# Optimization experiments

Hardware: AMD Instinct MI355X
Metric: run time of the kernel (lower is better)

Reference implementation:

```python
import jax, jax.numpy as jnp
import numpy as np

V, D, N, T, U, E = 200000, 128, 50000, 20, 128, 128

def setup_inputs() -> dict:
    key = jax.random.key(0)
    ks = jax.random.split(key, 12)
    s = 0.02
    return {
        "node_ids": jax.random.randint(ks[0], (N,), 0, V, dtype=jnp.int32),
        "neigh_ids": jax.random.randint(ks[1], (N, T), 0, V, dtype=jnp.int32),
        "alpha": jax.random.uniform(ks[2], (N, T), dtype=jnp.float32),
        "table": jax.random.normal(ks[3], (V, D), dtype=jnp.float32),
        "Wq": jax.random.normal(ks[4], (D, U), dtype=jnp.float32) * s,
        "bq": jnp.zeros((U,), dtype=jnp.float32),
        "Wn": jax.random.normal(ks[5], (D, U), dtype=jnp.float32) * s,
        "bn": jnp.zeros((U,), dtype=jnp.float32),
        "Ww": jax.random.normal(ks[6], (2 * U, U), dtype=jnp.float32) * s,
        "bw": jnp.zeros((U,), dtype=jnp.float32),
        "Wg": jax.random.normal(ks[7], (U, E), dtype=jnp.float32) * s,
        "bg": jnp.zeros((E,), dtype=jnp.float32),
    }

def reference(node_ids, neigh_ids, alpha, table, Wq, bq, Wn, bn, Ww, bw, Wg, bg):
    # gather initial embeddings (irregular indexing)
    node_x = table[node_ids]            # [N, D]
    neigh_x = table[neigh_ids]          # [N, T, D]
    # Convolve: node branch Dense+ReLU
    node_h = jax.nn.relu(node_x @ Wq + bq)                       # [N, U]
    # Aggregator: neighbor Dense+ReLU then alpha-weighted matmul
    neigh_h = jax.nn.relu(jnp.einsum('ntd,du->ntu', neigh_x, Wn) + bn)  # [N, T, U]
    agg = jnp.einsum('nt,ntu->nu', alpha, neigh_h)               # [N, U]
    # concat + Dense+ReLU
    emb = jax.nn.relu(jnp.concatenate([node_h, agg], axis=-1) @ Ww + bw)  # [N, U]
    # global (Frobenius) L2 normalize, as in tf.divide(Emb, tf.norm(Emb, ord=2))
    emb = emb / jnp.linalg.norm(emb)
    # final Dense+ReLU to emb_dim
    return jax.nn.relu(emb @ Wg + bg)                            # [N, E]
```

## Files before the change

### kernel.cpp

```cpp
#include <hip/hip_runtime.h>
#include <math.h>


using f32x4  = __attribute__((ext_vector_type(4))) float;
using short8 = __attribute__((ext_vector_type(8))) short;

__device__ __forceinline__ ushort f2bf(float f) {
    uint u = __float_as_uint(f);
    return (ushort)((u + 0x7fffu + ((u >> 16) & 1u)) >> 16);
}
__device__ __forceinline__ float bf2f(ushort h) {
    return __uint_as_float((uint)h << 16);
}
__device__ __forceinline__ uint pk2(float lo, float hi) {
    return (uint)f2bf(lo) | ((uint)f2bf(hi) << 16);
}
__device__ __forceinline__ short8 pack8(f32x4 a, f32x4 b) {
    uint4 r;
    r.x = pk2(a[0], a[1]); r.y = pk2(a[2], a[3]);
    r.z = pk2(b[0], b[1]); r.w = pk2(b[2], b[3]);
    union { uint4 u; short8 s; } cv; cv.u = r; return cv.s;
}

__global__ __launch_bounds__(256)
void prep_weights(const float* __restrict__ Wq, const float* __restrict__ Wn,
                  const float* __restrict__ Ww, const float* __restrict__ Wg,
                  ushort* __restrict__ WqT, ushort* __restrict__ WnT,
                  ushort* __restrict__ WwT, ushort* __restrict__ WgT)
{
    int idx = blockIdx.x * 256 + threadIdx.x;
    const float* W; ushort* WT; int K; int j = idx;
    if (j < 16384)      { W = Wq; WT = WqT; K = 128; }
    else if (j < 32768) { W = Wn; WT = WnT; K = 128; j -= 16384; }
    else if (j < 65536) { W = Ww; WT = WwT; K = 256; j -= 32768; }
    else                { W = Wg; WT = WgT; K = 128; j -= 65536; }
    int n = j & 127, k = j >> 7;
    WT[(size_t)n * K + k] = f2bf(W[j]);
}

__global__ __launch_bounds__(256, 2)
void k1_reg(const float* __restrict__ table, const int* __restrict__ node_ids,
            const ushort* __restrict__ WnT, const float* __restrict__ bn,
            const ushort* __restrict__ WqT, const float* __restrict__ bq,
            ushort* __restrict__ H, ushort* __restrict__ nh,
            int V, int N, int splitH)
{
    __shared__ float blds[128];
    const int tid = threadIdx.x;
    const int w = tid >> 6, l = tid & 63, l16 = l & 15, lh = l >> 4;
    const bool isH = (int)blockIdx.x < splitH;

    const ushort* WT = isH ? WnT : WqT;
    short8 wreg[4][8];
#pragma unroll
    for (int ks = 0; ks < 4; ++ks)
#pragma unroll
        for (int mt = 0; mt < 8; ++mt)
            wreg[ks][mt] = *reinterpret_cast<const short8*>(
                &WT[(size_t)(16 * mt + l16) * 128 + 32 * ks + 8 * lh]);
    if (tid < 128) blds[tid] = (isH ? bn : bq)[tid];
    __syncthreads();

    const int M   = isH ? V : N;
    ushort* out   = isH ? H : nh;
    const int ldo = isH ? 128 : 256;
    const int nt  = (M + 15) >> 4;
    const int wid    = (isH ? (int)blockIdx.x : (int)blockIdx.x - splitH) * 4 + w;
    const int nwaves = (isH ? splitH : (int)gridDim.x - splitH) * 4;

    for (int tile = wid; tile < nt; tile += nwaves) {
        const int row = tile * 16 + l16;
        int g = (row < M) ? row : (M - 1);
        if (!isH) g = node_ids[g];
        const float* rp = table + (size_t)g * 128 + 8 * lh;

        f32x4 f[8];
#pragma unroll
        for (int ks = 0; ks < 4; ++ks) {
            f[2 * ks]     = *reinterpret_cast<const f32x4*>(rp + 32 * ks);
            f[2 * ks + 1] = *reinterpret_cast<const f32x4*>(rp + 32 * ks + 4);
        }
        short8 a[4];
#pragma unroll
        for (int ks = 0; ks < 4; ++ks) a[ks] = pack8(f[2 * ks], f[2 * ks + 1]);

        f32x4 acc[8];
#pragma unroll
        for (int mt = 0; mt < 8; ++mt)
#pragma unroll
            for (int i = 0; i < 4; ++i) acc[mt][i] = 0.f;
#pragma unroll
        for (int ks = 0; ks < 4; ++ks)
#pragma unroll
            for (int mt = 0; mt < 8; ++mt)
                acc[mt] = __builtin_amdgcn_mfma_f32_16x16x32_bf16(
                    wreg[ks][mt], a[ks], acc[mt], 0, 0, 0);

        if (row < M) {
#pragma unroll
            for (int mt = 0; mt < 8; ++mt) {
                f32x4 bv = *reinterpret_cast<const f32x4*>(&blds[16 * mt + 4 * lh]);
                uint2 q;
                q.x = pk2(fmaxf(acc[mt][0] + bv[0], 0.f), fmaxf(acc[mt][1] + bv[1], 0.f));
                q.y = pk2(fmaxf(acc[mt][2] + bv[2], 0.f), fmaxf(acc[mt][3] + bv[3], 0.f));
                *reinterpret_cast<uint2*>(&out[(size_t)row * ldo + 16 * mt + 4 * lh]) = q;
            }
        }
    }
}

__global__ __launch_bounds__(256, 2)
void k5_reg(const ushort* __restrict__ embb, const ushort* __restrict__ WgT,
            const float* __restrict__ bg, const float* __restrict__ scale_ptr,
            float* __restrict__ outp, int N)
{
    __shared__ float blds[128];
    const int tid = threadIdx.x;
    const int w = tid >> 6, l = tid & 63, l16 = l & 15, lh = l >> 4;

    short8 wreg[4][8];
#pragma unroll
    for (int ks = 0; ks < 4; ++ks)
#pragma unroll
        for (int mt = 0; mt < 8; ++mt)
            wreg[ks][mt] = *reinterpret_cast<const short8*>(
                &WgT[(size_t)(16 * mt + l16) * 128 + 32 * ks + 8 * lh]);
    if (tid < 128) blds[tid] = bg[tid];
    __syncthreads();
    const float scale = scale_ptr[0];

    const int nt = (N + 15) >> 4;
    const int wid = (int)blockIdx.x * 4 + w;
    const int nwaves = (int)gridDim.x * 4;

    for (int tile = wid; tile < nt; tile += nwaves) {
        const int row = tile * 16 + l16;
        const int g = (row < N) ? row : (N - 1);
        const ushort* rp = embb + (size_t)g * 128 + 8 * lh;

        short8 a[4];
#pragma unroll
        for (int ks = 0; ks < 4; ++ks)
            a[ks] = *reinterpret_cast<const short8*>(rp + 32 * ks);

        f32x4 acc[8];
#pragma unroll
        for (int mt = 0; mt < 8; ++mt)
#pragma unroll
            for (int i = 0; i < 4; ++i) acc[mt][i] = 0.f;
#pragma unroll
        for (int ks = 0; ks < 4; ++ks)
#pragma unroll
            for (int mt = 0; mt < 8; ++mt)
                acc[mt] = __builtin_amdgcn_mfma_f32_16x16x32_bf16(
                    wreg[ks][mt], a[ks], acc[mt], 0, 0, 0);

        if (row < N) {
#pragma unroll
            for (int mt = 0; mt < 8; ++mt) {
                f32x4 bv = *reinterpret_cast<const f32x4*>(&blds[16 * mt + 4 * lh]);
                f32x4 v;
#pragma unroll
                for (int i = 0; i < 4; ++i)
                    v[i] = fmaxf(fmaf(acc[mt][i], scale, bv[i]), 0.f);
                *reinterpret_cast<f32x4*>(&outp[(size_t)row * 128 + 16 * mt + 4 * lh]) = v;
            }
        }
    }
}

__global__ __launch_bounds__(256)
void agg_bf16(const ushort* __restrict__ H,
              const int* __restrict__ nids,
              const float* __restrict__ alpha,
              ushort* __restrict__ outb,
              int N)
{
    const int n   = blockIdx.x * 16 + (threadIdx.x >> 4);
    const int l16 = threadIdx.x & 15;
    if (n >= N) return;

    const int*   idp = &nids[n * 20];
    const float* alp = &alpha[n * 20];
    float a[8];
#pragma unroll
    for (int j = 0; j < 8; ++j) a[j] = 0.f;
#pragma unroll
    for (int t = 0; t < 20; ++t) {
        const int   id = idp[t];
        const float al = alp[t];
        uint4 h = *reinterpret_cast<const uint4*>(&H[(size_t)id * 128 + 8 * l16]);
        a[0] = fmaf(al, bf2f((ushort)(h.x & 0xffff)), a[0]);
        a[1] = fmaf(al, bf2f((ushort)(h.x >> 16)),    a[1]);
        a[2] = fmaf(al, bf2f((ushort)(h.y & 0xffff)), a[2]);
        a[3] = fmaf(al, bf2f((ushort)(h.y >> 16)),    a[3]);
        a[4] = fmaf(al, bf2f((ushort)(h.z & 0xffff)), a[4]);
        a[5] = fmaf(al, bf2f((ushort)(h.z >> 16)),    a[5]);
        a[6] = fmaf(al, bf2f((ushort)(h.w & 0xffff)), a[6]);
        a[7] = fmaf(al, bf2f((ushort)(h.w >> 16)),    a[7]);
    }
    uint4 p;
    p.x = pk2(a[0], a[1]); p.y = pk2(a[2], a[3]);
    p.z = pk2(a[4], a[5]); p.w = pk2(a[6], a[7]);
    *reinterpret_cast<uint4*>(&outb[(size_t)n * 256 + 8 * l16]) = p;
}

__global__ __launch_bounds__(256, 2)
void k3_emb(const ushort* __restrict__ nh, const ushort* __restrict__ WT,
            const float* __restrict__ bias, ushort* __restrict__ embb,
            float* __restrict__ partials, int M)
{
    __shared__ __align__(16) char smem[65536];
    __shared__ float red[256];
    char* Bbase = smem + 32768;
    const int KTOT = 256, lda = 256, ldo = 128;

    const int tid = threadIdx.x;
    const int w   = tid >> 6;
    const int l   = tid & 63;
    const int l16 = l & 15, lh = l >> 4;
    const int brow = blockIdx.x * 128;

    f32x4 acc[2][8];
#pragma unroll
    for (int fr = 0; fr < 2; ++fr)
#pragma unroll
        for (int fc = 0; fc < 8; ++fc)
#pragma unroll
            for (int i = 0; i < 4; ++i) acc[fr][fc][i] = 0.f;

    for (int k0 = 0; k0 < KTOT; k0 += 128) {
#pragma unroll
        for (int it = 0; it < 8; ++it) {
            int idx = it * 256 + tid;
            int r = idx >> 4, o = idx & 15;
            int row = brow + r; int grow = (row < M) ? row : (M - 1);
            uint4 v = *reinterpret_cast<const uint4*>(&nh[(size_t)grow * lda + k0 + 8 * o]);
            *reinterpret_cast<uint4*>(smem + r * 256 + ((16 * o) ^ ((r & 7) << 4))) = v;
        }
#pragma unroll
        for (int it = 0; it < 8; ++it) {
            int idx = it * 256 + tid;
            int n = idx >> 4, o = idx & 15;
            uint4 v = *reinterpret_cast<const uint4*>(&WT[(size_t)n * KTOT + k0 + 8 * o]);
            *reinterpret_cast<uint4*>(Bbase + n * 256 + ((16 * o) ^ ((n & 7) << 4))) = v;
        }
        __syncthreads();

        const int r0 = 32 * w + l16;
        const int r1 = r0 + 16;
#pragma unroll
        for (int ks = 0; ks < 4; ++ks) {
            const int kb = 64 * ks + 16 * lh;
            short8 a0 = *reinterpret_cast<const short8*>(
                smem + r0 * 256 + (kb ^ ((r0 & 7) << 4)));
            short8 a1 = *reinterpret_cast<const short8*>(
                smem + r1 * 256 + (kb ^ ((r1 & 7) << 4)));
#pragma unroll
            for (int fc = 0; fc < 8; ++fc) {
                const int nn = 16 * fc + l16;
                short8 b = *reinterpret_cast<const short8*>(
                    Bbase + nn * 256 + (kb ^ ((nn & 7) << 4)));
                acc[0][fc] = __builtin_amdgcn_mfma_f32_16x16x32_bf16(a0, b, acc[0][fc], 0, 0, 0);
                acc[1][fc] = __builtin_amdgcn_mfma_f32_16x16x32_bf16(a1, b, acc[1][fc], 0, 0, 0);
            }
        }
        __syncthreads();
    }

    float bloc[8];
#pragma unroll
    for (int fc = 0; fc < 8; ++fc) bloc[fc] = bias[16 * fc + l16];

    float ssq = 0.f;
#pragma unroll
    for (int fr = 0; fr < 2; ++fr)
#pragma unroll
        for (int fc = 0; fc < 8; ++fc)
#pragma unroll
            for (int i = 0; i < 4; ++i) {
                const int r   = 32 * w + 16 * fr + 4 * lh + i;
                const int col = 16 * fc + l16;
                float v = fmaxf(acc[fr][fc][i] + bloc[fc], 0.f);
                if (brow + r < M) ssq += v * v;
                ((ushort*)smem)[r * 128 + col] = f2bf(v);
            }
    __syncthreads();

#pragma unroll
    for (int it = 0; it < 8; ++it) {
        int idx = it * 256 + tid;
        int r = idx >> 4, o = idx & 15;
        if (brow + r < M)
            *reinterpret_cast<uint4*>(&embb[(size_t)(brow + r) * ldo + 8 * o]) =
                *reinterpret_cast<const uint4*>((ushort*)smem + r * 128 + 8 * o);
    }

    red[tid] = ssq;
    __syncthreads();
    for (int st = 128; st > 0; st >>= 1) {
        if (tid < st) red[tid] += red[tid + st];
        __syncthreads();
    }
    if (tid == 0) partials[blockIdx.x] = red[0];
}

__global__ void reduce_norm(const float* __restrict__ partials, int n,
                            float* __restrict__ scale)
{
    __shared__ float red[256];
    float s = 0.f;
    for (int i = threadIdx.x; i < n; i += 256) s += partials[i];
    red[threadIdx.x] = s;
    __syncthreads();
    for (int st = 128; st > 0; st >>= 1) {
        if (threadIdx.x < st) red[threadIdx.x] += red[threadIdx.x + st];
        __syncthreads();
    }
    if (threadIdx.x == 0) scale[0] = 1.0f / sqrtf(red[0]);
}

extern "C" void kernel_launch(void* const* d_in, const int* in_sizes, int n_in,
                              void* d_out, int out_size, void* d_ws, size_t ws_size,
                              hipStream_t stream)
{
    const int*   node_ids  = (const int*)  d_in[0];
    const int*   neigh_ids = (const int*)  d_in[1];
    const float* alpha     = (const float*)d_in[2];
    const float* table     = (const float*)d_in[3];
    const float* Wq        = (const float*)d_in[4];
    const float* bq        = (const float*)d_in[5];
    const float* Wn        = (const float*)d_in[6];
    const float* bn        = (const float*)d_in[7];
    const float* Ww        = (const float*)d_in[8];
    const float* bw        = (const float*)d_in[9];
    const float* Wg        = (const float*)d_in[10];
    const float* bg        = (const float*)d_in[11];

    const int N = in_sizes[0];
    const int V = in_sizes[3] / 128;
    float* out = (float*)d_out;

    ushort* H    = (ushort*)d_ws;
    ushort* nh   = H    + (size_t)V * 128;
    ushort* embb = nh   + (size_t)N * 256;
    ushort* WqT  = embb + (size_t)N * 128;
    ushort* WnT  = WqT  + 16384;
    ushort* WwT  = WnT  + 16384;
    ushort* WgT  = WwT  + 32768;
    float*  partials = (float*)(WgT + 16384);
    float*  scale    = partials + 512;

    const size_t need = (size_t)((char*)(scale + 16) - (char*)d_ws);
    if (ws_size < need) return;

    const int nblkN = (N + 127) / 128;

    const int G1 = 512;
    const long long tH = (V + 15) / 16, tN = (N + 15) / 16;
    int splitH = (int)((G1 * tH) / (tH + tN));
    if (splitH < 1) splitH = 1;
    if (splitH > G1 - 1) splitH = G1 - 1;

    prep_weights<<<320, 256, 0, stream>>>(Wq, Wn, Ww, Wg, WqT, WnT, WwT, WgT);
    k1_reg<<<G1, 256, 0, stream>>>(table, node_ids, WnT, bn, WqT, bq,
                                   H, nh, V, N, splitH);
    agg_bf16<<<(N + 15) / 16, 256, 0, stream>>>(H, neigh_ids, alpha, nh + 128, N);
    k3_emb<<<nblkN, 256, 0, stream>>>(nh, WwT, bw, embb, partials, N);
    reduce_norm<<<1, 256, 0, stream>>>(partials, nblkN, scale);
    k5_reg<<<256, 256, 0, stream>>>(embb, WgT, bg, scale, out, N);
}
```

Measured before the change: 117.2 us.

## Software-prefetch next tile in GEMM kernels and fold norm reduction into final kernel

The k1 and final GEMM kernels now issue the global loads for the next tile before running the current tile's MFMAs, so memory latency overlaps with compute. Weight registers are pinned with an empty asm constraint so the compiler keeps them resident. The separate single-block reduce_norm launch is removed: every block of the final kernel re-reduces the ~391 partials itself. This saves one launch and a dependency gap, at the cost of redundant reduction work per block and higher register pressure from the prefetch buffers.

```diff
diff --git a/kernel.cpp b/kernel.cpp
--- a/kernel.cpp
+++ b/kernel.cpp
@@ -38,6 +38,23 @@
     WT[(size_t)n * K + k] = f2bf(W[j]);
 }
 
+__device__ __forceinline__ void load_wreg_pinned(const ushort* __restrict__ WT,
+                                                 short8 (&wreg)[4][8],
+                                                 int l16, int lh)
+{
+#pragma unroll
+    for (int ks = 0; ks < 4; ++ks)
+#pragma unroll
+        for (int mt = 0; mt < 8; ++mt)
+            wreg[ks][mt] = *reinterpret_cast<const short8*>(
+                &WT[(size_t)(16 * mt + l16) * 128 + 32 * ks + 8 * lh]);
+#pragma unroll
+    for (int ks = 0; ks < 4; ++ks)
+#pragma unroll
+        for (int mt = 0; mt < 8; ++mt)
+            asm volatile("" : "+v"(wreg[ks][mt]));
+}
+
 __global__ __launch_bounds__(256, 2)
 void k1_reg(const float* __restrict__ table, const int* __restrict__ node_ids,
             const ushort* __restrict__ WnT, const float* __restrict__ bn,
@@ -50,14 +67,8 @@
     const int w = tid >> 6, l = tid & 63, l16 = l & 15, lh = l >> 4;
     const bool isH = (int)blockIdx.x < splitH;
 
-    const ushort* WT = isH ? WnT : WqT;
     short8 wreg[4][8];
-#pragma unroll
-    for (int ks = 0; ks < 4; ++ks)
-#pragma unroll
-        for (int mt = 0; mt < 8; ++mt)
-            wreg[ks][mt] = *reinterpret_cast<const short8*>(
-                &WT[(size_t)(16 * mt + l16) * 128 + 32 * ks + 8 * lh]);
+    load_wreg_pinned(isH ? WnT : WqT, wreg, l16, lh);
     if (tid < 128) blds[tid] = (isH ? bn : bq)[tid];
     __syncthreads();
 
@@ -67,22 +78,38 @@
     const int nt  = (M + 15) >> 4;
     const int wid    = (isH ? (int)blockIdx.x : (int)blockIdx.x - splitH) * 4 + w;
     const int nwaves = (isH ? splitH : (int)gridDim.x - splitH) * 4;
-
-    for (int tile = wid; tile < nt; tile += nwaves) {
-        const int row = tile * 16 + l16;
+    if (wid >= nt) return;
+
+    f32x4 f[8];
+    {
+        const int row = wid * 16 + l16;
         int g = (row < M) ? row : (M - 1);
         if (!isH) g = node_ids[g];
         const float* rp = table + (size_t)g * 128 + 8 * lh;
-
-        f32x4 f[8];
 #pragma unroll
         for (int ks = 0; ks < 4; ++ks) {
             f[2 * ks]     = *reinterpret_cast<const f32x4*>(rp + 32 * ks);
             f[2 * ks + 1] = *reinterpret_cast<const f32x4*>(rp + 32 * ks + 4);
         }
+    }
+
+    for (int tile = wid; tile < nt; tile += nwaves) {
         short8 a[4];
 #pragma unroll
         for (int ks = 0; ks < 4; ++ks) a[ks] = pack8(f[2 * ks], f[2 * ks + 1]);
+
+        const int nxt = tile + nwaves;
+        if (nxt < nt) {
+            const int row = nxt * 16 + l16;
+            int g = (row < M) ? row : (M - 1);
+            if (!isH) g = node_ids[g];
+            const float* rp = table + (size_t)g * 128 + 8 * lh;
+#pragma unroll
+            for (int ks = 0; ks < 4; ++ks) {
+                f[2 * ks]     = *reinterpret_cast<const f32x4*>(rp + 32 * ks);
+                f[2 * ks + 1] = *reinterpret_cast<const f32x4*>(rp + 32 * ks + 4);
+            }
+        }
 
         f32x4 acc[8];
 #pragma unroll
@@ -96,6 +123,7 @@
                 acc[mt] = __builtin_amdgcn_mfma_f32_16x16x32_bf16(
                     wreg[ks][mt], a[ks], acc[mt], 0, 0, 0);
 
+        const int row = tile * 16 + l16;
         if (row < M) {
 #pragma unroll
             for (int mt = 0; mt < 8; ++mt) {
@@ -110,38 +138,61 @@
 }
 
 __global__ __launch_bounds__(256, 2)
-void k5_reg(const ushort* __restrict__ embb, const ushort* __restrict__ WgT,
-            const float* __restrict__ bg, const float* __restrict__ scale_ptr,
-            float* __restrict__ outp, int N)
+void k4_final(const ushort* __restrict__ embb, const ushort* __restrict__ WgT,
+              const float* __restrict__ bg, const float* __restrict__ partials,
+              int P, float* __restrict__ outp, int N)
 {
     __shared__ float blds[128];
+    __shared__ float red[256];
+    __shared__ float s_scale;
     const int tid = threadIdx.x;
     const int w = tid >> 6, l = tid & 63, l16 = l & 15, lh = l >> 4;
 
     short8 wreg[4][8];
-#pragma unroll
-    for (int ks = 0; ks < 4; ++ks)
-#pragma unroll
-        for (int mt = 0; mt < 8; ++mt)
-            wreg[ks][mt] = *reinterpret_cast<const short8*>(
-                &WgT[(size_t)(16 * mt + l16) * 128 + 32 * ks + 8 * lh]);
+    load_wreg_pinned(WgT, wreg, l16, lh);
     if (tid < 128) blds[tid] = bg[tid];
+
+    float s = 0.f;
+    for (int i = tid; i < P; i += 256) s += partials[i];
+    red[tid] = s;
     __syncthreads();
-    const float scale = scale_ptr[0];
+    for (int st = 128; st > 0; st >>= 1) {
+        if (tid < st) red[tid] += red[tid + st];
+        __syncthreads();
+    }
+    if (tid == 0) s_scale = 1.0f / sqrtf(red[0]);
+    __syncthreads();
+    const float scale = s_scale;
 
     const int nt = (N + 15) >> 4;
     const int wid = (int)blockIdx.x * 4 + w;
     const int nwaves = (int)gridDim.x * 4;
-
-    for (int tile = wid; tile < nt; tile += nwaves) {
-        const int row = tile * 16 + l16;
+    if (wid >= nt) return;
+
+    short8 a[4];
+    {
+        const int row = wid * 16 + l16;
         const int g = (row < N) ? row : (N - 1);
         const ushort* rp = embb + (size_t)g * 128 + 8 * lh;
-
-        short8 a[4];
 #pragma unroll
         for (int ks = 0; ks < 4; ++ks)
             a[ks] = *reinterpret_cast<const short8*>(rp + 32 * ks);
+    }
+
+    for (int tile = wid; tile < nt; tile += nwaves) {
+        short8 cur[4];
+#pragma unroll
+        for (int ks = 0; ks < 4; ++ks) cur[ks] = a[ks];
+
+        const int nxt = tile + nwaves;
+        if (nxt < nt) {
+            const int row = nxt * 16 + l16;
+            const int g = (row < N) ? row : (N - 1);
+            const ushort* rp = embb + (size_t)g * 128 + 8 * lh;
+#pragma unroll
+            for (int ks = 0; ks < 4; ++ks)
+                a[ks] = *reinterpret_cast<const short8*>(rp + 32 * ks);
+        }
 
         f32x4 acc[8];
 #pragma unroll
@@ -153,8 +204,9 @@
 #pragma unroll
             for (int mt = 0; mt < 8; ++mt)
                 acc[mt] = __builtin_amdgcn_mfma_f32_16x16x32_bf16(
-                    wreg[ks][mt], a[ks], acc[mt], 0, 0, 0);
-
+                    wreg[ks][mt], cur[ks], acc[mt], 0, 0, 0);
+
+        const int row = tile * 16 + l16;
         if (row < N) {
 #pragma unroll
             for (int mt = 0; mt < 8; ++mt) {
@@ -305,21 +357,6 @@
     if (tid == 0) partials[blockIdx.x] = red[0];
 }
 
-__global__ void reduce_norm(const float* __restrict__ partials, int n,
-                            float* __restrict__ scale)
-{
-    __shared__ float red[256];
-    float s = 0.f;
-    for (int i = threadIdx.x; i < n; i += 256) s += partials[i];
-    red[threadIdx.x] = s;
-    __syncthreads();
-    for (int st = 128; st > 0; st >>= 1) {
-        if (threadIdx.x < st) red[threadIdx.x] += red[threadIdx.x + st];
-        __syncthreads();
-    }
-    if (threadIdx.x == 0) scale[0] = 1.0f / sqrtf(red[0]);
-}
-
 extern "C" void kernel_launch(void* const* d_in, const int* in_sizes, int n_in,
                               void* d_out, int out_size, void* d_ws, size_t ws_size,
                               hipStream_t stream)
@@ -367,6 +404,5 @@
                                    H, nh, V, N, splitH);
     agg_bf16<<<(N + 15) / 16, 256, 0, stream>>>(H, neigh_ids, alpha, nh + 128, N);
     k3_emb<<<nblkN, 256, 0, stream>>>(nh, WwT, bw, embb, partials, N);
-    reduce_norm<<<1, 256, 0, stream>>>(partials, nblkN, scale);
-    k5_reg<<<256, 256, 0, stream>>>(embb, WgT, bg, scale, out, N);
-}
+    k4_final<<<256, 256, 0, stream>>>(embb, WgT, bg, partials, nblkN, out, N);
+}
```

After: 113.1 us. 3.5% less time.

## Stream fragment-ordered weights from cache instead of registers, fuse norm reduction into final GEMM

Applied to the files above, without the earlier changes.

Weights for the node/neighbor projections and the final dense layer are pre-packed into MFMA fragment order, so each lane reads contiguous short8 fragments from global/L2 per MFMA. This replaces the 32 short8 fragments each thread held in registers. The freed VGPRs allow launch bounds of 6 waves per SIMD and larger grids (1536 and 768 blocks), trading extra cached weight loads for higher occupancy and better latency hiding on the table gather. The separate single-block norm-reduction kernel is folded into the final GEMM, where every block redundantly sums the partials, saving one launch.

```diff
diff --git a/kernel.cpp b/kernel.cpp
--- a/kernel.cpp
+++ b/kernel.cpp
@@ -25,64 +25,63 @@
 __global__ __launch_bounds__(256)
 void prep_weights(const float* __restrict__ Wq, const float* __restrict__ Wn,
                   const float* __restrict__ Ww, const float* __restrict__ Wg,
-                  ushort* __restrict__ WqT, ushort* __restrict__ WnT,
-                  ushort* __restrict__ WwT, ushort* __restrict__ WgT)
-{
-    int idx = blockIdx.x * 256 + threadIdx.x;
-    const float* W; ushort* WT; int K; int j = idx;
-    if (j < 16384)      { W = Wq; WT = WqT; K = 128; }
-    else if (j < 32768) { W = Wn; WT = WnT; K = 128; j -= 16384; }
-    else if (j < 65536) { W = Ww; WT = WwT; K = 256; j -= 32768; }
-    else                { W = Wg; WT = WgT; K = 128; j -= 65536; }
-    int n = j & 127, k = j >> 7;
-    WT[(size_t)n * K + k] = f2bf(W[j]);
-}
-
-__global__ __launch_bounds__(256, 2)
-void k1_reg(const float* __restrict__ table, const int* __restrict__ node_ids,
-            const ushort* __restrict__ WnT, const float* __restrict__ bn,
-            const ushort* __restrict__ WqT, const float* __restrict__ bq,
-            ushort* __restrict__ H, ushort* __restrict__ nh,
-            int V, int N, int splitH)
-{
-    __shared__ float blds[128];
+                  ushort* __restrict__ WqF, ushort* __restrict__ WnF,
+                  ushort* __restrict__ WwT, ushort* __restrict__ WgF)
+{
+    int j = blockIdx.x * 256 + threadIdx.x;
+    if (j < 65536 && j >= 32768) {
+        int t = j - 32768;
+        int n = t & 127, k = t >> 7;
+        WwT[(size_t)n * 256 + k] = f2bf(Ww[t]);
+        return;
+    }
+    const float* W; ushort* WF;
+    int e_out = j;
+    if (j < 16384)      { W = Wq; WF = WqF; }
+    else if (j < 32768) { W = Wn; WF = WnF; e_out -= 16384; }
+    else                { W = Wg; WF = WgF; e_out -= 65536; }
+    int c = e_out >> 3, e = e_out & 7;
+    int mtks = c >> 6, lane = c & 63;
+    int ks = mtks >> 3, mt = mtks & 7;
+    int l16 = lane & 15, lh = lane >> 4;
+    WF[e_out] = f2bf(W[(size_t)(32 * ks + 8 * lh + e) * 128 + 16 * mt + l16]);
+}
+
+__global__ __launch_bounds__(256, 6)
+void k1_nolds(const float* __restrict__ table, const int* __restrict__ node_ids,
+              const ushort* __restrict__ WnF, const float* __restrict__ bn,
+              const ushort* __restrict__ WqF, const float* __restrict__ bq,
+              ushort* __restrict__ H, ushort* __restrict__ nh,
+              int V, int N, int splitH)
+{
     const int tid = threadIdx.x;
     const int w = tid >> 6, l = tid & 63, l16 = l & 15, lh = l >> 4;
     const bool isH = (int)blockIdx.x < splitH;
 
-    const ushort* WT = isH ? WnT : WqT;
-    short8 wreg[4][8];
-#pragma unroll
-    for (int ks = 0; ks < 4; ++ks)
-#pragma unroll
-        for (int mt = 0; mt < 8; ++mt)
-            wreg[ks][mt] = *reinterpret_cast<const short8*>(
-                &WT[(size_t)(16 * mt + l16) * 128 + 32 * ks + 8 * lh]);
-    if (tid < 128) blds[tid] = (isH ? bn : bq)[tid];
-    __syncthreads();
-
+    const ushort* WF   = isH ? WnF : WqF;
+    const float*  bias = isH ? bn : bq;
     const int M   = isH ? V : N;
     ushort* out   = isH ? H : nh;
     const int ldo = isH ? 128 : 256;
     const int nt  = (M + 15) >> 4;
-    const int wid    = (isH ? (int)blockIdx.x : (int)blockIdx.x - splitH) * 4 + w;
-    const int nwaves = (isH ? splitH : (int)gridDim.x - splitH) * 4;
-
-    for (int tile = wid; tile < nt; tile += nwaves) {
+    const int wid = (isH ? (int)blockIdx.x : (int)blockIdx.x - splitH) * 4 + w;
+    const int nwv = (isH ? splitH : (int)gridDim.x - splitH) * 4;
+
+    const ushort* wbase = WF + (size_t)l * 8;
+
+    for (int tile = wid; tile < nt; tile += nwv) {
         const int row = tile * 16 + l16;
         int g = (row < M) ? row : (M - 1);
         if (!isH) g = node_ids[g];
         const float* rp = table + (size_t)g * 128 + 8 * lh;
 
-        f32x4 f[8];
+        short8 a[4];
 #pragma unroll
         for (int ks = 0; ks < 4; ++ks) {
-            f[2 * ks]     = *reinterpret_cast<const f32x4*>(rp + 32 * ks);
-            f[2 * ks + 1] = *reinterpret_cast<const f32x4*>(rp + 32 * ks + 4);
-        }
-        short8 a[4];
-#pragma unroll
-        for (int ks = 0; ks < 4; ++ks) a[ks] = pack8(f[2 * ks], f[2 * ks + 1]);
+            f32x4 c0 = *reinterpret_cast<const f32x4*>(rp + 32 * ks);
+            f32x4 c1 = *reinterpret_cast<const f32x4*>(rp + 32 * ks + 4);
+            a[ks] = pack8(c0, c1);
+        }
 
         f32x4 acc[8];
 #pragma unroll
@@ -92,78 +91,20 @@
 #pragma unroll
         for (int ks = 0; ks < 4; ++ks)
 #pragma unroll
-            for (int mt = 0; mt < 8; ++mt)
-                acc[mt] = __builtin_amdgcn_mfma_f32_16x16x32_bf16(
-                    wreg[ks][mt], a[ks], acc[mt], 0, 0, 0);
+            for (int mt = 0; mt < 8; ++mt) {
+                short8 wf = *reinterpret_cast<const short8*>(
+                    wbase + (size_t)(ks * 8 + mt) * 512);
+                acc[mt] = __builtin_amdgcn_mfma_f32_16x16x32_bf16(wf, a[ks], acc[mt], 0, 0, 0);
+            }
 
         if (row < M) {
 #pragma unroll
             for (int mt = 0; mt < 8; ++mt) {
-                f32x4 bv = *reinterpret_cast<const f32x4*>(&blds[16 * mt + 4 * lh]);
+                f32x4 bv = *reinterpret_cast<const f32x4*>(&bias[16 * mt + 4 * lh]);
                 uint2 q;
                 q.x = pk2(fmaxf(acc[mt][0] + bv[0], 0.f), fmaxf(acc[mt][1] + bv[1], 0.f));
                 q.y = pk2(fmaxf(acc[mt][2] + bv[2], 0.f), fmaxf(acc[mt][3] + bv[3], 0.f));
                 *reinterpret_cast<uint2*>(&out[(size_t)row * ldo + 16 * mt + 4 * lh]) = q;
-            }
-        }
-    }
-}
-
-__global__ __launch_bounds__(256, 2)
-void k5_reg(const ushort* __restrict__ embb, const ushort* __restrict__ WgT,
-            const float* __restrict__ bg, const float* __restrict__ scale_ptr,
-            float* __restrict__ outp, int N)
-{
-    __shared__ float blds[128];
-    const int tid = threadIdx.x;
-    const int w = tid >> 6, l = tid & 63, l16 = l & 15, lh = l >> 4;
-
-    short8 wreg[4][8];
-#pragma unroll
-    for (int ks = 0; ks < 4; ++ks)
-#pragma unroll
-        for (int mt = 0; mt < 8; ++mt)
-            wreg[ks][mt] = *reinterpret_cast<const short8*>(
-                &WgT[(size_t)(16 * mt + l16) * 128 + 32 * ks + 8 * lh]);
-    if (tid < 128) blds[tid] = bg[tid];
-    __syncthreads();
-    const float scale = scale_ptr[0];
-
-    const int nt = (N + 15) >> 4;
-    const int wid = (int)blockIdx.x * 4 + w;
-    const int nwaves = (int)gridDim.x * 4;
-
-    for (int tile = wid; tile < nt; tile += nwaves) {
-        const int row = tile * 16 + l16;
-        const int g = (row < N) ? row : (N - 1);
-        const ushort* rp = embb + (size_t)g * 128 + 8 * lh;
-
-        short8 a[4];
-#pragma unroll
-        for (int ks = 0; ks < 4; ++ks)
-            a[ks] = *reinterpret_cast<const short8*>(rp + 32 * ks);
-
-        f32x4 acc[8];
-#pragma unroll
-        for (int mt = 0; mt < 8; ++mt)
-#pragma unroll
-            for (int i = 0; i < 4; ++i) acc[mt][i] = 0.f;
-#pragma unroll
-        for (int ks = 0; ks < 4; ++ks)
-#pragma unroll
-            for (int mt = 0; mt < 8; ++mt)
-                acc[mt] = __builtin_amdgcn_mfma_f32_16x16x32_bf16(
-                    wreg[ks][mt], a[ks], acc[mt], 0, 0, 0);
-
-        if (row < N) {
-#pragma unroll
-            for (int mt = 0; mt < 8; ++mt) {
-                f32x4 bv = *reinterpret_cast<const f32x4*>(&blds[16 * mt + 4 * lh]);
-                f32x4 v;
-#pragma unroll
-                for (int i = 0; i < 4; ++i)
-                    v[i] = fmaxf(fmaf(acc[mt][i], scale, bv[i]), 0.f);
-                *reinterpret_cast<f32x4*>(&outp[(size_t)row * 128 + 16 * mt + 4 * lh]) = v;
             }
         }
     }
@@ -305,19 +246,69 @@
     if (tid == 0) partials[blockIdx.x] = red[0];
 }
 
-__global__ void reduce_norm(const float* __restrict__ partials, int n,
-                            float* __restrict__ scale)
+__global__ __launch_bounds__(256, 6)
+void k5_final(const ushort* __restrict__ embb, const ushort* __restrict__ WgF,
+              const float* __restrict__ bg, const float* __restrict__ partials,
+              int P, float* __restrict__ outp, int N)
 {
     __shared__ float red[256];
+    __shared__ float s_scale;
+    const int tid = threadIdx.x;
+    const int w = tid >> 6, l = tid & 63, l16 = l & 15, lh = l >> 4;
+
     float s = 0.f;
-    for (int i = threadIdx.x; i < n; i += 256) s += partials[i];
-    red[threadIdx.x] = s;
+    for (int i = tid; i < P; i += 256) s += partials[i];
+    red[tid] = s;
     __syncthreads();
     for (int st = 128; st > 0; st >>= 1) {
-        if (threadIdx.x < st) red[threadIdx.x] += red[threadIdx.x + st];
+        if (tid < st) red[tid] += red[tid + st];
         __syncthreads();
     }
-    if (threadIdx.x == 0) scale[0] = 1.0f / sqrtf(red[0]);
+    if (tid == 0) s_scale = 1.0f / sqrtf(red[0]);
+    __syncthreads();
+    const float scale = s_scale;
+
+    const int nt = (N + 15) >> 4;
+    const int wid = (int)blockIdx.x * 4 + w;
+    const int nwv = (int)gridDim.x * 4;
+    const ushort* wbase = WgF + (size_t)l * 8;
+
+    for (int tile = wid; tile < nt; tile += nwv) {
+        const int row = tile * 16 + l16;
+        const int g = (row < N) ? row : (N - 1);
+        const ushort* rp = embb + (size_t)g * 128 + 8 * lh;
+
+        short8 a[4];
+#pragma unroll
+        for (int ks = 0; ks < 4; ++ks)
+            a[ks] = *reinterpret_cast<const short8*>(rp + 32 * ks);
+
+        f32x4 acc[8];
+#pragma unroll
+        for (int mt = 0; mt < 8; ++mt)
+#pragma unroll
+            for (int i = 0; i < 4; ++i) acc[mt][i] = 0.f;
+#pragma unroll
+        for (int ks = 0; ks < 4; ++ks)
+#pragma unroll
+            for (int mt = 0; mt < 8; ++mt) {
+                short8 wf = *reinterpret_cast<const short8*>(
+                    wbase + (size_t)(ks * 8 + mt) * 512);
+                acc[mt] = __builtin_amdgcn_mfma_f32_16x16x32_bf16(wf, a[ks], acc[mt], 0, 0, 0);
+            }
+
+        if (row < N) {
+#pragma unroll
+            for (int mt = 0; mt < 8; ++mt) {
+                f32x4 bv = *reinterpret_cast<const f32x4*>(&bg[16 * mt + 4 * lh]);
+                f32x4 v;
+#pragma unroll
+                for (int i = 0; i < 4; ++i)
+                    v[i] = fmaxf(fmaf(acc[mt][i], scale, bv[i]), 0.f);
+                *reinterpret_cast<f32x4*>(&outp[(size_t)row * 128 + 16 * mt + 4 * lh]) = v;
+            }
+        }
+    }
 }
 
 extern "C" void kernel_launch(void* const* d_in, const int* in_sizes, int n_in,
@@ -344,11 +335,11 @@
     ushort* H    = (ushort*)d_ws;
     ushort* nh   = H    + (size_t)V * 128;
     ushort* embb = nh   + (size_t)N * 256;
-    ushort* WqT  = embb + (size_t)N * 128;
-    ushort* WnT  = WqT  + 16384;
-    ushort* WwT  = WnT  + 16384;
-    ushort* WgT  = WwT  + 32768;
-    float*  partials = (float*)(WgT + 16384);
+    ushort* WqF  = embb + (size_t)N * 128;
+    ushort* WnF  = WqF  + 16384;
+    ushort* WwT  = WnF  + 16384;
+    ushort* WgF  = WwT  + 32768;
+    float*  partials = (float*)(WgF + 16384);
     float*  scale    = partials + 512;
 
     const size_t need = (size_t)((char*)(scale + 16) - (char*)d_ws);
@@ -356,17 +347,16 @@
 
     const int nblkN = (N + 127) / 128;
 
-    const int G1 = 512;
+    const int G1 = 1536;
     const long long tH = (V + 15) / 16, tN = (N + 15) / 16;
     int splitH = (int)((G1 * tH) / (tH + tN));
     if (splitH < 1) splitH = 1;
     if (splitH > G1 - 1) splitH = G1 - 1;
 
-    prep_weights<<<320, 256, 0, stream>>>(Wq, Wn, Ww, Wg, WqT, WnT, WwT, WgT);
-    k1_reg<<<G1, 256, 0, stream>>>(table, node_ids, WnT, bn, WqT, bq,
-                                   H, nh, V, N, splitH);
+    prep_weights<<<320, 256, 0, stream>>>(Wq, Wn, Ww, Wg, WqF, WnF, WwT, WgF);
+    k1_nolds<<<G1, 256, 0, stream>>>(table, node_ids, WnF, bn, WqF, bq,
+                                     H, nh, V, N, splitH);
     agg_bf16<<<(N + 15) / 16, 256, 0, stream>>>(H, neigh_ids, alpha, nh + 128, N);
     k3_emb<<<nblkN, 256, 0, stream>>>(nh, WwT, bw, embb, partials, N);
-    reduce_norm<<<1, 256, 0, stream>>>(partials, nblkN, scale);
-    k5_reg<<<256, 256, 0, stream>>>(embb, WgT, bg, scale, out, N);
-}
+    k5_final<<<768, 256, 0, stream>>>(embb, WgF, bg, partials, nblkN, out, N);
+}
```

New measurement: 269.7 us. 2.3x slower.
